# Kernel optimization log

Hardware: AMD Instinct MI355X
Metric: run time of the kernel (lower is better)

Reference implementation:

```python
import jax, jax.numpy as jnp
import numpy as np
import math

NC = 80              # num classes
NA = 18              # 3 anchor shapes x 6 angles
NCH = 5 + 1 + NC     # x,y,w,h,a,conf,cls...
STRIDES = [8, 16]
SXY = [1.2, 1.1]
ANCH = [[[10, 13], [16, 30], [33, 23]], [[30, 61], [62, 45], [59, 119]]]
RAD = math.pi / 180.0
ANGLES = [RAD * a for a in (-60.0, -30.0, 0.0, 30.0, 60.0, 90.0)]


def _masked_anchors(level):
    s = STRIDES[level]
    return jnp.array([[w / s, h / s, a] for (w, h) in ANCH[level] for a in ANGLES],
                     dtype=jnp.float32)  # [18, 3]


def _decode(feat, W, b, level):
    # feat: [B, C, G, G], W: [out_ch, C], b: [out_ch]
    B, C, G, _ = feat.shape
    out = jnp.einsum('bchw,oc->bohw', feat, W) + b[None, :, None, None]  # 1x1 conv
    pred = out.reshape(B, NA, NCH, G, G).transpose(0, 1, 3, 4, 2)  # [B, A, gy, gx, NCH]
    sxy = SXY[level]
    s = float(STRIDES[level])
    ma = _masked_anchors(level)
    aw = ma[:, 0][None, :, None, None]
    ah = ma[:, 1][None, :, None, None]
    aa = ma[:, 2][None, :, None, None]
    gx = jnp.arange(G, dtype=pred.dtype)[None, None, None, :]
    gy = jnp.arange(G, dtype=pred.dtype)[None, None, :, None]
    px = jax.nn.sigmoid(pred[..., 0]) * sxy - (sxy - 1.0) / 2.0 + gx
    py = jax.nn.sigmoid(pred[..., 1]) * sxy - (sxy - 1.0) / 2.0 + gy
    pw = jnp.exp(pred[..., 2]) * aw
    ph = jnp.exp(pred[..., 3]) * ah
    pa = pred[..., 4] + aa
    conf = jax.nn.sigmoid(pred[..., 5])
    cls = jax.nn.sigmoid(pred[..., 6:])
    boxes = jnp.stack([px * s, py * s, pw * s, ph * s, pa], axis=-1)  # xywh scaled, angle raw
    out = jnp.concatenate([boxes, conf[..., None], cls], axis=-1)
    return out.reshape(B, -1, NCH)


def setup_inputs() -> dict:
    key = jax.random.key(0)
    k = jax.random.split(key, 6)
    return {
        'x0': jax.random.normal(k[0], (8, 256, 64, 64), dtype=jnp.float32),
        'x1': jax.random.normal(k[1], (8, 512, 32, 32), dtype=jnp.float32),
        'W0': jax.random.normal(k[2], (1548, 256), dtype=jnp.float32) * 0.02,
        'b0': jnp.zeros((1548,), dtype=jnp.float32),
        'W1': jax.random.normal(k[3], (1548, 512), dtype=jnp.float32) * 0.02,
        'b1': jnp.zeros((1548,), dtype=jnp.float32),
    }


def reference(x0, x1, W0, b0, W1, b1):
    o0 = _decode(x0, W0, b0, 0)  # [B, 18*64*64, 86]
    o1 = _decode(x1, W1, b1, 1)  # [B, 18*32*32, 86]
    return jnp.concatenate([o0, o1], axis=1)
```

## Files before the change

### kernel.cpp

```cpp
#include <hip/hip_runtime.h>
#include <hip/hip_bf16.h>


typedef __attribute__((ext_vector_type(8))) short short8;
typedef __attribute__((ext_vector_type(4))) short short4v;
typedef __attribute__((ext_vector_type(4))) float f32x4;
typedef unsigned int u32;

__device__ __forceinline__ unsigned short f2bf(float f) {
    union { float f; unsigned u; } c; c.f = f;
    return (unsigned short)((c.u + 0x7fffu + ((c.u >> 16) & 1u)) >> 16);
}
__device__ __forceinline__ float sigm(float v) {
    return 1.0f / (1.0f + __expf(-v));
}
__device__ __forceinline__ void gload16(const void* g, void* l) {
    __builtin_amdgcn_global_load_lds(
        (const __attribute__((address_space(1))) u32*)g,
        (__attribute__((address_space(3))) u32*)l, 16, 0, 0);
}

#define OUT_CH 1548
#define NCHN   86
#define BPB    7925760


__global__ void conv_w_kernel(const float* __restrict__ W0, unsigned short* __restrict__ Wb0,
                              const float* __restrict__ W1, unsigned short* __restrict__ Wb1) {
    int i = blockIdx.x * blockDim.x + threadIdx.x;
    if (i >= 297216) return;
    const float* W = W0;
    unsigned short* Wb = Wb0;
    if (i >= 99072) { W = W1; Wb = Wb1; i -= 99072; }
    const float4 f = ((const float4*)W)[i];
    short4v v;
    v[0] = (short)f2bf(f.x); v[1] = (short)f2bf(f.y);
    v[2] = (short)f2bf(f.z); v[3] = (short)f2bf(f.w);
    ((short4v*)Wb)[i] = v;
}

__global__ void transpose_x_kernel(const float* __restrict__ X, unsigned short* __restrict__ Xb,
                                   int C, int GG) {
    __shared__ float sT[64][65];
    const int p0 = blockIdx.x * 64;
    const int c0 = blockIdx.y * 64;
    const int b  = blockIdx.z;
    const int tid = threadIdx.x;
    const float* src = X + ((size_t)b * C + c0) * GG + p0;
    const int rc = tid >> 4;
    const int cp = (tid & 15) * 4;
    #pragma unroll
    for (int rr = 0; rr < 4; ++rr) {
        const int c = rc + rr * 16;
        const float4 f = *(const float4*)&src[(size_t)c * GG + cp];
        sT[c][cp + 0] = f.x; sT[c][cp + 1] = f.y;
        sT[c][cp + 2] = f.z; sT[c][cp + 3] = f.w;
    }
    __syncthreads();
    const int p  = tid >> 2;
    const int cg = (tid & 3) * 16;
    unsigned short u[16];
    #pragma unroll
    for (int k = 0; k < 16; ++k) u[k] = f2bf(sT[cg + k][p]);
    unsigned short* dst = Xb + ((size_t)b * GG + p0 + p) * C + c0 + cg;
    *(short8*)dst       = *(const short8*)&u[0];
    *(short8*)(dst + 8) = *(const short8*)&u[8];
}


__global__ __launch_bounds__(512, 8) void detect_gemm(
    const unsigned short* __restrict__ Xb0, const unsigned short* __restrict__ Xb1,
    const unsigned short* __restrict__ Wb0, const unsigned short* __restrict__ Wb1,
    const float* __restrict__ b0, const float* __restrict__ b1,
    float* __restrict__ out)
{
    __shared__ __attribute__((aligned(128))) char smem[40960];
    unsigned short* sAbase = (unsigned short*)smem;
    unsigned short* sBbase = (unsigned short*)(smem + 16384);
    float* sOutF = (float*)smem;

    const int bid = blockIdx.x;
    const int v   = (bid & 7) * 1440 + (bid >> 3);
    const int mt  = v / 18;
    const int a   = v - mt * 18;

    const bool lvl1 = (mt >= 512);
    const unsigned short* __restrict__ Xb = lvl1 ? Xb1 : Xb0;
    const unsigned short* __restrict__ Wb = lvl1 ? Wb1 : Wb0;
    const float* __restrict__ biasA = (lvl1 ? b1 : b0) + a * NCHN;
    const int C   = lvl1 ? 512 : 256;
    const int GG  = lvl1 ? 1024 : 4096;
    const int Gsh = lvl1 ? 5 : 6;
    const float sxy     = lvl1 ? 1.1f : 1.2f;
    const float sxy_off = (sxy - 1.0f) * 0.5f;
    const float sf      = lvl1 ? 16.0f : 8.0f;
    const int shp  = a / 6;
    const int angi = a - shp * 6;
    const float aw = lvl1 ? ((shp == 0) ? 30.f : (shp == 1) ? 62.f : 59.f)
                          : ((shp == 0) ? 10.f : (shp == 1) ? 16.f : 33.f);
    const float ah = lvl1 ? ((shp == 0) ? 61.f : (shp == 1) ? 45.f : 119.f)
                          : ((shp == 0) ? 13.f : (shp == 1) ? 30.f : 23.f);
    const float aa = (angi == 0) ? -1.04719755119659775f :
                     (angi == 1) ? -0.52359877559829887f :
                     (angi == 2) ?  0.0f :
                     (angi == 3) ?  0.52359877559829887f :
                     (angi == 4) ?  1.04719755119659775f :
                                    1.57079632679489662f;

    const int tloc = lvl1 ? (mt - 512) : mt;
    const int b  = tloc >> (lvl1 ? 4 : 6);
    const int p0 = (tloc & ((lvl1 ? 16 : 64) - 1)) * 64;

    const unsigned short* __restrict__ Xp = Xb + ((size_t)b * GG + p0) * C;

    const int tid  = threadIdx.x;
    const int lane = tid & 63;
    const int wid  = tid >> 6;
    const int wm = wid >> 1;
    const int wn = wid & 1;

    f32x4 acc[3];
    #pragma unroll
    for (int j = 0; j < 3; ++j)
        acc[j] = f32x4{0.f, 0.f, 0.f, 0.f};

    const int rowIn = lane >> 3;
    const int scolE = ((((lane & 7) << 4)) ^ (rowIn << 4)) >> 1;

    const int lr   = lane & 15;
    const int kqb  = (lane >> 4) << 4;
    const int swzR = (lr & 7) << 4;

    const int KT = C >> 6;

    auto stage = [&](int bufsel, int kt) {
        const int k0 = kt << 6;
        unsigned short* sA = sAbase + bufsel * 4096;
        unsigned short* sB = sBbase + bufsel * 6144;
        {
            const int row = wid * 8 + rowIn;
            gload16(Xp + (size_t)row * C + k0 + scolE, (char*)sA + wid * 1024);
        }
        {
            const int n = wid * 8 + rowIn;
            int grow = a * NCHN + n;
            grow = grow > (OUT_CH - 1) ? (OUT_CH - 1) : grow;
            gload16(Wb + (size_t)grow * C + k0 + scolE, (char*)sB + wid * 1024);
        }
        if (wid < 4) {
            const int n = 64 + wid * 8 + rowIn;
            int grow = a * NCHN + n;
            grow = grow > (OUT_CH - 1) ? (OUT_CH - 1) : grow;
            gload16(Wb + (size_t)grow * C + k0 + scolE, (char*)sB + 8192 + wid * 1024);
        }
    };

    auto compute = [&](int bufsel) {
        const unsigned short* sA = sAbase + bufsel * 4096;
        const unsigned short* sB = sBbase + bufsel * 6144;
        #pragma unroll
        for (int kk = 0; kk < 2; ++kk) {
            const int cb = (kk << 6) + kqb;
            const int ra = wm * 16 + lr;
            const short8 af = *(const short8*)((const char*)sA + ra * 128 + (cb ^ swzR));
            short8 bfr[3];
            #pragma unroll
            for (int j = 0; j < 3; ++j) {
                const int rb = wn * 48 + j * 16 + lr;
                bfr[j] = *(const short8*)((const char*)sB + rb * 128 + (cb ^ swzR));
            }
            #pragma unroll
            for (int j = 0; j < 3; ++j)
                acc[j] = __builtin_amdgcn_mfma_f32_16x16x32_bf16(af, bfr[j], acc[j], 0, 0, 0);
        }
    };

    stage(0, 0);
    __syncthreads();
    int cur = 0;
    for (int kt = 0; kt < KT; ++kt) {
        if (kt + 1 < KT) stage(cur ^ 1, kt + 1);
        compute(cur);
        __syncthreads();
        cur ^= 1;
    }

    const int rq = (lane >> 4) * 4;
    const int lvloff = lvl1 ? 73728 : 0;

    #pragma unroll
    for (int j = 0; j < 3; ++j) {
        const int ch = wn * 48 + j * 16 + lr;
        if (ch < NCHN) {
            const float bv = biasA[ch];
            #pragma unroll
            for (int r = 0; r < 4; ++r) {
                const int px = wm * 16 + rq + r;
                const int p  = p0 + px;
                const float vv = acc[j][r] + bv;
                float res;
                if (ch == 0)      res = (sigm(vv) * sxy - sxy_off + (float)(p & ((1 << Gsh) - 1))) * sf;
                else if (ch == 1) res = (sigm(vv) * sxy - sxy_off + (float)(p >> Gsh)) * sf;
                else if (ch == 2) res = __expf(vv) * aw;
                else if (ch == 3) res = __expf(vv) * ah;
                else if (ch == 4) res = vv + aa;
                else              res = sigm(vv);
                sOutF[px * NCHN + ch] = res;
            }
        }
    }
    __syncthreads();

    const size_t spanDw = (size_t)b * BPB + ((size_t)(lvloff + a * GG + p0)) * NCHN;
    #pragma unroll
    for (int k = 0; k < 3; ++k) {
        const int f4 = tid + k * 512;
        if (f4 < 1376) {
            const f32x4 vv = *(const f32x4*)&sOutF[f4 * 4];
            __builtin_nontemporal_store(vv, (f32x4*)&out[spanDw + f4 * 4]);
        }
    }
}

extern "C" void kernel_launch(void* const* d_in, const int* in_sizes, int n_in,
                              void* d_out, int out_size, void* d_ws, size_t ws_size,
                              hipStream_t stream) {
    const float* x0 = (const float*)d_in[0];
    const float* x1 = (const float*)d_in[1];
    const float* W0 = (const float*)d_in[2];
    const float* b0 = (const float*)d_in[3];
    const float* W1 = (const float*)d_in[4];
    const float* b1 = (const float*)d_in[5];
    float* out = (float*)d_out;

    constexpr size_t XB0_OFF = 0;
    constexpr size_t XB1_OFF = 16777216;
    constexpr size_t WB0_OFF = 25165824;
    constexpr size_t WB1_OFF = 25958400;

    unsigned short* Xb0 = (unsigned short*)((char*)d_ws + XB0_OFF);
    unsigned short* Xb1 = (unsigned short*)((char*)d_ws + XB1_OFF);
    unsigned short* Wb0 = (unsigned short*)((char*)d_ws + WB0_OFF);
    unsigned short* Wb1 = (unsigned short*)((char*)d_ws + WB1_OFF);

    hipLaunchKernelGGL(conv_w_kernel, dim3((297216 + 255) / 256), dim3(256), 0, stream,
                       W0, Wb0, W1, Wb1);
    hipLaunchKernelGGL(transpose_x_kernel, dim3(64, 4, 8), dim3(256), 0, stream,
                       x0, Xb0, 256, 4096);
    hipLaunchKernelGGL(transpose_x_kernel, dim3(16, 8, 8), dim3(256), 0, stream,
                       x1, Xb1, 512, 1024);

    hipLaunchKernelGGL(detect_gemm, dim3(11520), dim3(512), 0, stream,
                       Xb0, Xb1, Wb0, Wb1, b0, b1, out);
}
```

Baseline: 149.5 us.

## Triple-buffer GEMM K-loop with manual vmcnt waits and one barrier per step

Replaces the double-buffered LDS pipeline with a three-stage ring, prefetching two K-tiles ahead. It waits with explicit s_waitcnt vmcnt counts and one s_barrier per iteration instead of a full __syncthreads after each compute. The B-tile load is now issued by all waves without the wid<4 branch, and the row indices are hoisted out of the loop. LDS grows from 40 KB to 72 KB and launch bounds drop from 8 to 4 blocks, so occupancy falls in exchange for deeper latency hiding.

```diff
diff --git a/kernel.cpp b/kernel.cpp
--- a/kernel.cpp
+++ b/kernel.cpp
@@ -68,15 +68,13 @@
 }
 
 
-__global__ __launch_bounds__(512, 8) void detect_gemm(
+__global__ __launch_bounds__(512, 4) void detect_gemm(
     const unsigned short* __restrict__ Xb0, const unsigned short* __restrict__ Xb1,
     const unsigned short* __restrict__ Wb0, const unsigned short* __restrict__ Wb1,
     const float* __restrict__ b0, const float* __restrict__ b1,
     float* __restrict__ out)
 {
-    __shared__ __attribute__((aligned(128))) char smem[40960];
-    unsigned short* sAbase = (unsigned short*)smem;
-    unsigned short* sBbase = (unsigned short*)(smem + 16384);
+    __shared__ __attribute__((aligned(128))) char smem[73728];
     float* sOutF = (float*)smem;
 
     const int bid = blockIdx.x;
@@ -133,41 +131,32 @@
 
     const int KT = C >> 6;
 
+    const int nB1 = a * NCHN + wid * 8 + rowIn;
+    const int nB2 = nB1 + 64;
+    const int gB1 = nB1 > (OUT_CH - 1) ? (OUT_CH - 1) : nB1;
+    const int gB2 = nB2 > (OUT_CH - 1) ? (OUT_CH - 1) : nB2;
+    const int rowA = wid * 8 + rowIn;
+
     auto stage = [&](int bufsel, int kt) {
         const int k0 = kt << 6;
-        unsigned short* sA = sAbase + bufsel * 4096;
-        unsigned short* sB = sBbase + bufsel * 6144;
-        {
-            const int row = wid * 8 + rowIn;
-            gload16(Xp + (size_t)row * C + k0 + scolE, (char*)sA + wid * 1024);
-        }
-        {
-            const int n = wid * 8 + rowIn;
-            int grow = a * NCHN + n;
-            grow = grow > (OUT_CH - 1) ? (OUT_CH - 1) : grow;
-            gload16(Wb + (size_t)grow * C + k0 + scolE, (char*)sB + wid * 1024);
-        }
-        if (wid < 4) {
-            const int n = 64 + wid * 8 + rowIn;
-            int grow = a * NCHN + n;
-            grow = grow > (OUT_CH - 1) ? (OUT_CH - 1) : grow;
-            gload16(Wb + (size_t)grow * C + k0 + scolE, (char*)sB + 8192 + wid * 1024);
-        }
+        char* base = smem + bufsel * 24576;
+        gload16(Xp + (size_t)rowA * C + k0 + scolE, base + wid * 1024);
+        gload16(Wb + (size_t)gB1 * C + k0 + scolE, base + 8192 + wid * 1024);
+        gload16(Wb + (size_t)gB2 * C + k0 + scolE, base + 16384 + wid * 1024);
     };
 
     auto compute = [&](int bufsel) {
-        const unsigned short* sA = sAbase + bufsel * 4096;
-        const unsigned short* sB = sBbase + bufsel * 6144;
+        const char* base = smem + bufsel * 24576;
         #pragma unroll
         for (int kk = 0; kk < 2; ++kk) {
             const int cb = (kk << 6) + kqb;
             const int ra = wm * 16 + lr;
-            const short8 af = *(const short8*)((const char*)sA + ra * 128 + (cb ^ swzR));
+            const short8 af = *(const short8*)(base + ra * 128 + (cb ^ swzR));
             short8 bfr[3];
             #pragma unroll
             for (int j = 0; j < 3; ++j) {
                 const int rb = wn * 48 + j * 16 + lr;
-                bfr[j] = *(const short8*)((const char*)sB + rb * 128 + (cb ^ swzR));
+                bfr[j] = *(const short8*)(base + 8192 + rb * 128 + (cb ^ swzR));
             }
             #pragma unroll
             for (int j = 0; j < 3; ++j)
@@ -176,14 +165,18 @@
     };
 
     stage(0, 0);
+    if (KT > 1) stage(1, 1);
+    for (int kt = 0; kt < KT; ++kt) {
+        if (kt < KT - 1) {
+            asm volatile("s_waitcnt vmcnt(3)" ::: "memory");
+        } else {
+            asm volatile("s_waitcnt vmcnt(0)" ::: "memory");
+        }
+        __builtin_amdgcn_s_barrier();
+        if (kt + 2 < KT) stage((kt + 2) % 3, kt + 2);
+        compute(kt % 3);
+    }
     __syncthreads();
-    int cur = 0;
-    for (int kt = 0; kt < KT; ++kt) {
-        if (kt + 1 < KT) stage(cur ^ 1, kt + 1);
-        compute(cur);
-        __syncthreads();
-        cur ^= 1;
-    }
 
     const int rq = (lane >> 4) * 4;
     const int lvloff = lvl1 ? 73728 : 0;
```

Measured after the change: 186.8 us. +25.0%, slower.

## Keep X tile resident in LDS and loop over six anchors per block

Applied to the files above, without the earlier changes.

Each block now loads its 64-pixel activation tile into LDS once and computes six anchors against it, streaming the weight slices through a double-buffered pipeline with explicit vmcnt waits. The goal is to stop re-reading the same X tile from global memory for every anchor and to cut the block count from 11520 to 1920. The epilogue is split into two 32-pixel halves so the staging buffer fits alongside the resident tile. LDS use rises to about 69KB, which limits occupancy to two blocks per CU, and the hand-written waitcnt/barrier schedule is fragile.

```diff
diff --git a/kernel.cpp b/kernel.cpp
--- a/kernel.cpp
+++ b/kernel.cpp
@@ -18,6 +18,20 @@
     __builtin_amdgcn_global_load_lds(
         (const __attribute__((address_space(1))) u32*)g,
         (__attribute__((address_space(3))) u32*)l, 16, 0, 0);
+}
+__device__ __forceinline__ void waitv(int n) {
+    switch (n) {
+    case 0:  asm volatile("s_waitcnt vmcnt(0)" ::: "memory"); break;
+    case 1:  asm volatile("s_waitcnt vmcnt(1)" ::: "memory"); break;
+    case 2:  asm volatile("s_waitcnt vmcnt(2)" ::: "memory"); break;
+    case 3:  asm volatile("s_waitcnt vmcnt(3)" ::: "memory"); break;
+    case 4:  asm volatile("s_waitcnt vmcnt(4)" ::: "memory"); break;
+    case 6:  asm volatile("s_waitcnt vmcnt(6)" ::: "memory"); break;
+    case 7:  asm volatile("s_waitcnt vmcnt(7)" ::: "memory"); break;
+    case 8:  asm volatile("s_waitcnt vmcnt(8)" ::: "memory"); break;
+    default: asm volatile("s_waitcnt vmcnt(10)" ::: "memory"); break;
+    }
+    __builtin_amdgcn_sched_barrier(0);
 }
 
 #define OUT_CH 1548
@@ -68,158 +82,205 @@
 }
 
 
-__global__ __launch_bounds__(512, 8) void detect_gemm(
+template<int LVL>
+__device__ __forceinline__ void body(int v, char* smem,
+    const unsigned short* __restrict__ Xb, const unsigned short* __restrict__ Wb,
+    const float* __restrict__ bias, float* __restrict__ out)
+{
+    constexpr int C    = LVL ? 512 : 256;
+    constexpr int GG   = LVL ? 1024 : 4096;
+    constexpr int Gsh  = LVL ? 5 : 6;
+    constexpr int KT   = LVL ? 8 : 4;
+    constexpr int S    = 6 * KT;
+    constexpr int LVOF = LVL ? 73728 : 0;
+    const float sxy     = LVL ? 1.1f : 1.2f;
+    const float sxy_off = (sxy - 1.0f) * 0.5f;
+    const float sf      = LVL ? 16.0f : 8.0f;
+
+    unsigned short* sA = (unsigned short*)smem;
+    char* sB0   = smem + 32768;
+    float* sImg = (float*)(smem + 57344);
+    float* sBias= (float*)(smem + 68352);
+
+    const int m   = v / 3;
+    const int grp = v - m * 3;
+    const int aBase = grp * 6;
+    const int b  = m >> (LVL ? 4 : 6);
+    const int p0 = (m & (LVL ? 15 : 63)) * 64;
+
+    const int tid  = threadIdx.x;
+    const int lane = tid & 63;
+    const int wid  = tid >> 6;
+    const int wm = wid >> 1;
+    const int wn = wid & 1;
+    const int lr  = lane & 15;
+    const int kqb = (lane >> 4) << 4;
+    const int rq  = (lane >> 4) * 4;
+    const int swzR = (lr & 7) << 4;
+
+    const unsigned short* __restrict__ Xp = Xb + ((size_t)b * GG + p0) * C;
+
+    const int rowInA = tid >> 5;
+    const int colAe  = ((((tid & 31) << 4)) ^ ((rowInA & 7) << 4)) >> 1;
+    const int rowInB = lane >> 3;
+    const int colBe  = ((((lane & 7) << 4)) ^ ((rowInB & 7) << 4)) >> 1;
+
+    auto stageA = [&](int h) {
+        #pragma unroll
+        for (int i = 0; i < 4; ++i)
+            gload16(Xp + (size_t)(i * 16 + rowInA) * C + h * 256 + colAe,
+                    smem + i * 8192 + tid * 16);
+    };
+    auto stageB = [&](int s) {
+        const int ag = aBase + (s >> (LVL ? 3 : 2));
+        const int k0 = (s & (KT - 1)) << 6;
+        char* dst = sB0 + (s & 1) * 12288;
+        {
+            const int row = wid * 8 + rowInB;
+            int grow = ag * NCHN + row;
+            grow = grow > (OUT_CH - 1) ? (OUT_CH - 1) : grow;
+            gload16(Wb + (size_t)grow * C + k0 + colBe, dst + wid * 1024);
+        }
+        if (wid < 4) {
+            const int row = 64 + wid * 8 + rowInB;
+            int grow = ag * NCHN + row;
+            grow = grow > (OUT_CH - 1) ? (OUT_CH - 1) : grow;
+            gload16(Wb + (size_t)grow * C + k0 + colBe, dst + 8192 + wid * 1024);
+        }
+    };
+
+    f32x4 acc[3];
+    #pragma unroll
+    for (int j = 0; j < 3; ++j) acc[j] = f32x4{0.f, 0.f, 0.f, 0.f};
+
+    auto compute = [&](int buf, int kt) {
+        const char* bb = sB0 + buf * 12288;
+        const int colbase = (kt & 3) << 7;
+        #pragma unroll
+        for (int kk = 0; kk < 2; ++kk) {
+            const int cbA = (colbase + (kk << 6) + kqb) ^ swzR;
+            const int cbB = (((kk << 6) + kqb)) ^ swzR;
+            const int ra = wm * 16 + lr;
+            const short8 af = *(const short8*)((const char*)sA + ra * 512 + cbA);
+            short8 bfr[3];
+            #pragma unroll
+            for (int j = 0; j < 3; ++j) {
+                const int rb = wn * 48 + j * 16 + lr;
+                bfr[j] = *(const short8*)(bb + rb * 128 + cbB);
+            }
+            #pragma unroll
+            for (int j = 0; j < 3; ++j)
+                acc[j] = __builtin_amdgcn_mfma_f32_16x16x32_bf16(af, bfr[j], acc[j], 0, 0, 0);
+        }
+    };
+
+    auto epilogue = [&](int aL) {
+        const int ag = aBase + aL;
+        const int shp  = ag / 6;
+        const int angi = ag - shp * 6;
+        const float aw = LVL ? ((shp == 0) ? 30.f : (shp == 1) ? 62.f : 59.f)
+                             : ((shp == 0) ? 10.f : (shp == 1) ? 16.f : 33.f);
+        const float ah = LVL ? ((shp == 0) ? 61.f : (shp == 1) ? 45.f : 119.f)
+                             : ((shp == 0) ? 13.f : (shp == 1) ? 30.f : 23.f);
+        const float aa = (angi == 0) ? -1.04719755119659775f :
+                         (angi == 1) ? -0.52359877559829887f :
+                         (angi == 2) ?  0.0f :
+                         (angi == 3) ?  0.52359877559829887f :
+                         (angi == 4) ?  1.04719755119659775f :
+                                        1.57079632679489662f;
+        const size_t span = (size_t)b * BPB + ((size_t)(LVOF + ag * GG + p0)) * NCHN;
+        #pragma unroll
+        for (int h = 0; h < 2; ++h) {
+            if ((wid >> 2) == h) {
+                #pragma unroll
+                for (int j = 0; j < 3; ++j) {
+                    const int ch = wn * 48 + j * 16 + lr;
+                    if (ch < NCHN) {
+                        const float bv = sBias[aL * NCHN + ch];
+                        #pragma unroll
+                        for (int r = 0; r < 4; ++r) {
+                            const int px = wm * 16 + rq + r;
+                            const int pl = px - h * 32;
+                            const int p  = p0 + px;
+                            const float vv = acc[j][r] + bv;
+                            float res;
+                            if (ch == 0)      res = (sigm(vv) * sxy - sxy_off + (float)(p & ((1 << Gsh) - 1))) * sf;
+                            else if (ch == 1) res = (sigm(vv) * sxy - sxy_off + (float)(p >> Gsh)) * sf;
+                            else if (ch == 2) res = __expf(vv) * aw;
+                            else if (ch == 3) res = __expf(vv) * ah;
+                            else if (ch == 4) res = vv + aa;
+                            else              res = sigm(vv);
+                            sImg[pl * NCHN + ch] = res;
+                        }
+                    }
+                }
+            }
+            asm volatile("s_waitcnt lgkmcnt(0)" ::: "memory");
+            __builtin_amdgcn_sched_barrier(0);
+            __builtin_amdgcn_s_barrier();
+            const size_t base = span + (size_t)h * 32 * NCHN;
+            #pragma unroll
+            for (int k = 0; k < 2; ++k) {
+                const int f4 = tid + k * 512;
+                if (f4 < 688) {
+                    const f32x4 vv = *(const f32x4*)&sImg[f4 * 4];
+                    __builtin_nontemporal_store(vv, (f32x4*)&out[base + (size_t)f4 * 4]);
+                }
+            }
+            __builtin_amdgcn_s_barrier();
+        }
+        #pragma unroll
+        for (int j = 0; j < 3; ++j) acc[j] = f32x4{0.f, 0.f, 0.f, 0.f};
+    };
+
+    {
+        float bv0 = bias[aBase * NCHN + tid];
+        sBias[tid] = bv0;
+        if (tid < 4) sBias[512 + tid] = bias[aBase * NCHN + 512 + tid];
+    }
+    stageA(0);
+    stageB(0);
+    stageB(1);
+    asm volatile("s_waitcnt vmcnt(0) lgkmcnt(0)" ::: "memory");
+    __builtin_amdgcn_sched_barrier(0);
+    __builtin_amdgcn_s_barrier();
+
+    for (int aL = 0; aL < 6; ++aL) {
+        for (int kt = 0; kt < KT; ++kt) {
+            const int s = aL * KT + kt;
+            int wn_;
+            if (s >= S - 1)      wn_ = 0;
+            else if (kt == 0) {
+                if (aL == 0)     wn_ = 0;
+                else if (!LVL)   wn_ = (wid < 3) ? 6 : (wid < 4) ? 4 : 3;
+                else             wn_ = (wid < 3) ? 10 : (wid < 4) ? 8 : 7;
+            } else               wn_ = (wid < 4) ? 2 : 1;
+            waitv(wn_);
+            __builtin_amdgcn_s_barrier();
+            compute(s & 1, kt);
+            __builtin_amdgcn_s_barrier();
+            if (kt == KT - 1) {
+                if (LVL && aL < 5) stageA(0);
+                epilogue(aL);
+            } else if (LVL && kt == 3) {
+                stageA(1);
+            }
+            if (s + 2 < S) stageB(s + 2);
+        }
+    }
+}
+
+__global__ __launch_bounds__(512, 2) void detect_gemm(
     const unsigned short* __restrict__ Xb0, const unsigned short* __restrict__ Xb1,
     const unsigned short* __restrict__ Wb0, const unsigned short* __restrict__ Wb1,
     const float* __restrict__ b0, const float* __restrict__ b1,
     float* __restrict__ out)
 {
-    __shared__ __attribute__((aligned(128))) char smem[40960];
-    unsigned short* sAbase = (unsigned short*)smem;
-    unsigned short* sBbase = (unsigned short*)(smem + 16384);
-    float* sOutF = (float*)smem;
-
+    __shared__ __attribute__((aligned(128))) char smem[70656];
     const int bid = blockIdx.x;
-    const int v   = (bid & 7) * 1440 + (bid >> 3);
-    const int mt  = v / 18;
-    const int a   = v - mt * 18;
-
-    const bool lvl1 = (mt >= 512);
-    const unsigned short* __restrict__ Xb = lvl1 ? Xb1 : Xb0;
-    const unsigned short* __restrict__ Wb = lvl1 ? Wb1 : Wb0;
-    const float* __restrict__ biasA = (lvl1 ? b1 : b0) + a * NCHN;
-    const int C   = lvl1 ? 512 : 256;
-    const int GG  = lvl1 ? 1024 : 4096;
-    const int Gsh = lvl1 ? 5 : 6;
-    const float sxy     = lvl1 ? 1.1f : 1.2f;
-    const float sxy_off = (sxy - 1.0f) * 0.5f;
-    const float sf      = lvl1 ? 16.0f : 8.0f;
-    const int shp  = a / 6;
-    const int angi = a - shp * 6;
-    const float aw = lvl1 ? ((shp == 0) ? 30.f : (shp == 1) ? 62.f : 59.f)
-                          : ((shp == 0) ? 10.f : (shp == 1) ? 16.f : 33.f);
-    const float ah = lvl1 ? ((shp == 0) ? 61.f : (shp == 1) ? 45.f : 119.f)
-                          : ((shp == 0) ? 13.f : (shp == 1) ? 30.f : 23.f);
-    const float aa = (angi == 0) ? -1.04719755119659775f :
-                     (angi == 1) ? -0.52359877559829887f :
-                     (angi == 2) ?  0.0f :
-                     (angi == 3) ?  0.52359877559829887f :
-                     (angi == 4) ?  1.04719755119659775f :
-                                    1.57079632679489662f;
-
-    const int tloc = lvl1 ? (mt - 512) : mt;
-    const int b  = tloc >> (lvl1 ? 4 : 6);
-    const int p0 = (tloc & ((lvl1 ? 16 : 64) - 1)) * 64;
-
-    const unsigned short* __restrict__ Xp = Xb + ((size_t)b * GG + p0) * C;
-
-    const int tid  = threadIdx.x;
-    const int lane = tid & 63;
-    const int wid  = tid >> 6;
-    const int wm = wid >> 1;
-    const int wn = wid & 1;
-
-    f32x4 acc[3];
-    #pragma unroll
-    for (int j = 0; j < 3; ++j)
-        acc[j] = f32x4{0.f, 0.f, 0.f, 0.f};
-
-    const int rowIn = lane >> 3;
-    const int scolE = ((((lane & 7) << 4)) ^ (rowIn << 4)) >> 1;
-
-    const int lr   = lane & 15;
-    const int kqb  = (lane >> 4) << 4;
-    const int swzR = (lr & 7) << 4;
-
-    const int KT = C >> 6;
-
-    auto stage = [&](int bufsel, int kt) {
-        const int k0 = kt << 6;
-        unsigned short* sA = sAbase + bufsel * 4096;
-        unsigned short* sB = sBbase + bufsel * 6144;
-        {
-            const int row = wid * 8 + rowIn;
-            gload16(Xp + (size_t)row * C + k0 + scolE, (char*)sA + wid * 1024);
-        }
-        {
-            const int n = wid * 8 + rowIn;
-            int grow = a * NCHN + n;
-            grow = grow > (OUT_CH - 1) ? (OUT_CH - 1) : grow;
-            gload16(Wb + (size_t)grow * C + k0 + scolE, (char*)sB + wid * 1024);
-        }
-        if (wid < 4) {
-            const int n = 64 + wid * 8 + rowIn;
-            int grow = a * NCHN + n;
-            grow = grow > (OUT_CH - 1) ? (OUT_CH - 1) : grow;
-            gload16(Wb + (size_t)grow * C + k0 + scolE, (char*)sB + 8192 + wid * 1024);
-        }
-    };
-
-    auto compute = [&](int bufsel) {
-        const unsigned short* sA = sAbase + bufsel * 4096;
-        const unsigned short* sB = sBbase + bufsel * 6144;
-        #pragma unroll
-        for (int kk = 0; kk < 2; ++kk) {
-            const int cb = (kk << 6) + kqb;
-            const int ra = wm * 16 + lr;
-            const short8 af = *(const short8*)((const char*)sA + ra * 128 + (cb ^ swzR));
-            short8 bfr[3];
-            #pragma unroll
-            for (int j = 0; j < 3; ++j) {
-                const int rb = wn * 48 + j * 16 + lr;
-                bfr[j] = *(const short8*)((const char*)sB + rb * 128 + (cb ^ swzR));
-            }
-            #pragma unroll
-            for (int j = 0; j < 3; ++j)
-                acc[j] = __builtin_amdgcn_mfma_f32_16x16x32_bf16(af, bfr[j], acc[j], 0, 0, 0);
-        }
-    };
-
-    stage(0, 0);
-    __syncthreads();
-    int cur = 0;
-    for (int kt = 0; kt < KT; ++kt) {
-        if (kt + 1 < KT) stage(cur ^ 1, kt + 1);
-        compute(cur);
-        __syncthreads();
-        cur ^= 1;
-    }
-
-    const int rq = (lane >> 4) * 4;
-    const int lvloff = lvl1 ? 73728 : 0;
-
-    #pragma unroll
-    for (int j = 0; j < 3; ++j) {
-        const int ch = wn * 48 + j * 16 + lr;
-        if (ch < NCHN) {
-            const float bv = biasA[ch];
-            #pragma unroll
-            for (int r = 0; r < 4; ++r) {
-                const int px = wm * 16 + rq + r;
-                const int p  = p0 + px;
-                const float vv = acc[j][r] + bv;
-                float res;
-                if (ch == 0)      res = (sigm(vv) * sxy - sxy_off + (float)(p & ((1 << Gsh) - 1))) * sf;
-                else if (ch == 1) res = (sigm(vv) * sxy - sxy_off + (float)(p >> Gsh)) * sf;
-                else if (ch == 2) res = __expf(vv) * aw;
-                else if (ch == 3) res = __expf(vv) * ah;
-                else if (ch == 4) res = vv + aa;
-                else              res = sigm(vv);
-                sOutF[px * NCHN + ch] = res;
-            }
-        }
-    }
-    __syncthreads();
-
-    const size_t spanDw = (size_t)b * BPB + ((size_t)(lvloff + a * GG + p0)) * NCHN;
-    #pragma unroll
-    for (int k = 0; k < 3; ++k) {
-        const int f4 = tid + k * 512;
-        if (f4 < 1376) {
-            const f32x4 vv = *(const f32x4*)&sOutF[f4 * 4];
-            __builtin_nontemporal_store(vv, (f32x4*)&out[spanDw + f4 * 4]);
-        }
-    }
+    const int v   = (bid & 7) * 240 + (bid >> 3);
+    if (v < 1536) body<0>(v,        smem, Xb0, Wb0, b0, out);
+    else          body<1>(v - 1536, smem, Xb1, Wb1, b1, out);
 }
 
 extern "C" void kernel_launch(void* const* d_in, const int* in_sizes, int n_in,
@@ -250,6 +311,6 @@
     hipLaunchKernelGGL(transpose_x_kernel, dim3(16, 8, 8), dim3(256), 0, stream,
                        x1, Xb1, 512, 1024);
 
-    hipLaunchKernelGGL(detect_gemm, dim3(11520), dim3(512), 0, stream,
+    hipLaunchKernelGGL(detect_gemm, dim3(1920), dim3(512), 0, stream,
                        Xb0, Xb1, Wb0, Wb1, b0, b1, out);
 }
```

New measurement: 244.0 us. +63.2%, slower.
